# Kernel optimization log

Hardware: AMD Instinct MI355X
Metric: run time of the kernel (lower is better)

Reference implementation:

```python
import jax, jax.numpy as jnp
import numpy as np

N_COMP = 4        # config.n_components (num_cell_anchors = 1)
C = 256           # FPN channel width
ANCHOR_SCALE = 8.0  # anchor side = stride * 8 (single cell anchor per location)


def _conv(x, w, b, pad):
    y = jax.lax.conv_general_dilated(x, w, (1, 1), [(pad, pad), (pad, pad)],
                                     dimension_numbers=('NCHW', 'OIHW', 'NCHW'))
    return y + b[None, :, None, None]


def _anchors(H, W, stride):
    ys = (jnp.arange(H, dtype=jnp.float32) + 0.5) * stride
    xs = (jnp.arange(W, dtype=jnp.float32) + 0.5) * stride
    cy, cx = jnp.meshgrid(ys, xs, indexing='ij')
    s = stride * ANCHOR_SCALE * 0.5
    return jnp.stack([cx - s, cy - s, cx + s, cy + s], -1).reshape(-1, 4)


def _decode(anchors, deltas):
    # anchors [N,4] xyxy, deltas [B,N,4] -> boxes [B,N,4]
    aw = anchors[:, 2] - anchors[:, 0]
    ah = anchors[:, 3] - anchors[:, 1]
    acx = (anchors[:, 0] + anchors[:, 2]) * 0.5
    acy = (anchors[:, 1] + anchors[:, 3]) * 0.5
    cx = acx + deltas[..., 0] * aw
    cy = acy + deltas[..., 1] * ah
    bw = aw * jnp.exp(jnp.clip(deltas[..., 2], -10.0, 10.0))
    bh = ah * jnp.exp(jnp.clip(deltas[..., 3], -10.0, 10.0))
    return jnp.stack([cx - bw * 0.5, cy - bh * 0.5, cx + bw * 0.5, cy + bh * 0.5], -1)


def _forward(feats, im_info, w_qy1, b_qy1, w_qy2, b_qy2, w_qy, b_qy,
             w_rpn, b_rpn, w_cls, b_cls, w_mean, b_mean):
    strides = [64.0, 32.0, 16.0, 8.0, 4.0]  # off_stride = 2**(L-1) halving per level, base_stride=4
    outs = []
    for x, stride in zip(feats, strides):
        h = jax.nn.relu(_conv(x, w_qy1, b_qy1, 1))
        h = jax.nn.relu(_conv(h, w_qy2, b_qy2, 1))
        qy = _conv(h, w_qy, b_qy, 1)                 # [B, K, H, W]
        mix = jax.nn.softmax(qy, axis=1)             # per-location component weights
        bb_c, sc_c = [], []
        for n in range(N_COMP):
            # one-hot component indicator map concatenated onto the feature
            y = jnp.zeros_like(qy).at[:, n].set(1.0)
            t = jax.nn.relu(_conv(jnp.concatenate([x, y], axis=1), w_rpn, b_rpn, 1))
            sc_c.append(_conv(t, w_cls, b_cls, 0))    # [B,2,H,W]
            bb_c.append(_conv(t, w_mean, b_mean, 0))  # [B,4,H,W]; eval: bbox = mean
        # find_top_rpn_gmm_box: combine components with qy softmax weights
        bb = (mix[:, :, None] * jnp.stack(bb_c, 1)).sum(1)   # [B,4,H,W]
        sc = (mix[:, :, None] * jnp.stack(sc_c, 1)).sum(1)   # [B,2,H,W]
        B, _, H, W = bb.shape
        deltas = bb.transpose(0, 2, 3, 1).reshape(B, H * W, 4)
        scores = sc.transpose(0, 2, 3, 1).reshape(B, H * W, 2)
        boxes = _decode(_anchors(H, W, stride), deltas)
        lim = jnp.stack([im_info[:, 1], im_info[:, 0], im_info[:, 1], im_info[:, 0]], -1)[:, None, :]
        boxes = jnp.clip(boxes, 0.0, lim)             # clip to image
        outs.append(jnp.concatenate([boxes, scores], -1))
    return jnp.concatenate(outs, axis=1)  # [B, sum(H*W), 6]


def setup_inputs() -> dict:
    key = jax.random.key(0)
    ks = jax.random.split(key, 12)
    fshapes = [(2, C, 13, 19), (2, C, 25, 38), (2, C, 50, 76), (2, C, 100, 152), (2, C, 200, 304)]
    inp = {f"feat{i}": jax.random.normal(ks[i], s, jnp.float32) for i, s in enumerate(fshapes)}
    inp["im_info"] = jnp.tile(jnp.array([[800.0, 1216.0, 1.0, 800.0, 1216.0, 1.0]], jnp.float32), (2, 1))
    std = 0.01
    inp["w_qy1"] = jax.random.normal(ks[5], (C, C, 3, 3), jnp.float32) * std
    inp["b_qy1"] = jnp.zeros((C,), jnp.float32)
    inp["w_qy2"] = jax.random.normal(ks[6], (C, C, 3, 3), jnp.float32) * std
    inp["b_qy2"] = jnp.zeros((C,), jnp.float32)
    inp["w_qy"] = jax.random.normal(ks[7], (N_COMP, C, 3, 3), jnp.float32) * std
    inp["b_qy"] = jnp.zeros((N_COMP,), jnp.float32)
    inp["w_rpn"] = jax.random.normal(ks[8], (C, C + N_COMP, 3, 3), jnp.float32) * std
    inp["b_rpn"] = jnp.zeros((C,), jnp.float32)
    inp["w_cls"] = jax.random.normal(ks[9], (2, C, 1, 1), jnp.float32) * std
    inp["b_cls"] = jnp.zeros((2,), jnp.float32)
    inp["w_mean"] = jax.random.normal(ks[10], (4, C, 1, 1), jnp.float32) * std
    inp["b_mean"] = jnp.zeros((4,), jnp.float32)
    return inp


def reference(feat0, feat1, feat2, feat3, feat4, im_info,
              w_qy1, b_qy1, w_qy2, b_qy2, w_qy, b_qy,
              w_rpn, b_rpn, w_cls, b_cls, w_mean, b_mean):
    return _forward([feat0, feat1, feat2, feat3, feat4], im_info,
                    w_qy1, b_qy1, w_qy2, b_qy2, w_qy, b_qy,
                    w_rpn, b_rpn, w_cls, b_cls, w_mean, b_mean)
```

## Files before the change

kernel.cpp:

```cpp
#include <hip/hip_runtime.h>
#include <math.h>


typedef __attribute__((ext_vector_type(8))) short short8;
typedef __attribute__((ext_vector_type(4))) float f32x4;

#define TOT 80997

struct Tab {
    int tilesX[5];
    int blkBase[6];
    int H[5];
    int W5[5];
    int poff[6];
    int cvtBase[6];
};

static __device__ __forceinline__ ushort f2bf(float f) {
    union { float f; unsigned u; } x; x.f = f;
    unsigned r = (x.u + 0x7FFFu + ((x.u >> 16) & 1u)) >> 16;
    return (ushort)r;
}
static __device__ __forceinline__ float bf2f(ushort u) {
    union { unsigned u; float f; } x; x.u = ((unsigned)u) << 16;
    return x.f;
}

static __device__ __forceinline__ void gl_lds16(const ushort* g, ushort* l) {
    __builtin_amdgcn_global_load_lds(
        (const __attribute__((address_space(1))) void*)g,
        (__attribute__((address_space(3))) void*)l, 16, 0, 0);
}

__global__ __launch_bounds__(256) void cvtT_kernel(
    const float* __restrict__ f0, const float* __restrict__ f1,
    const float* __restrict__ f2, const float* __restrict__ f3,
    const float* __restrict__ f4, ushort* __restrict__ xn, Tab tab)
{
    __shared__ __align__(16) ushort s[64 * 264];
    const int tid = threadIdx.x;
    int t = blockIdx.x, L = 0;
    while (t >= tab.cvtBase[L + 1]) ++L;
    const int tile = t - tab.cvtBase[L];
    const int HW = tab.H[L] * tab.W5[L];
    const int pos0 = tile * 64;
    const int b = blockIdx.z;
    const float* fs[5] = {f0, f1, f2, f3, f4};
    const float* xp = fs[L] + (size_t)b * 256 * HW;

    const int p = tid & 63;
    const int icr = tid >> 6;
    const int pos = pos0 + p;
    for (int ic4 = 0; ic4 < 256; ic4 += 4) {
        const int ic = ic4 + icr;
        float v = 0.f;
        if (pos < HW) v = xp[(size_t)ic * HW + pos];
        s[p * 264 + ic] = f2bf(v);
    }
    __syncthreads();
    const int seg = tid & 31;
    for (int k = 0; k < 8; ++k) {
        const int pp = (tid >> 5) + k * 8;
        const int gpos = pos0 + pp;
        if (gpos < HW) {
            short8 v = *(const short8*)&s[pp * 264 + seg * 8];
            __builtin_nontemporal_store(v,
                (short8*)(xn + ((size_t)b * TOT + tab.poff[L] + gpos) * 256 + seg * 8));
        }
    }
}

__global__ __launch_bounds__(256) void pack_w_kernel(
    const float* __restrict__ w, ushort* __restrict__ pw, int icfull)
{
    int idx = blockIdx.x * 256 + threadIdx.x;
    if (idx >= 589824) return;
    const int within = idx & 511;
    const int lm  = within >> 5;
    const int qe  = within & 31;
    const int rest = idx >> 9;
    const int ocg = rest & 15;
    const int tc  = rest >> 4;
    const int c   = tc & 7;
    const int tap = tc >> 3;
    const int oc = ocg * 16 + lm;
    const int ic = c * 32 + qe;
    pw[idx] = f2bf(w[((size_t)oc * icfull + ic) * 9 + tap]);
}

__global__ __launch_bounds__(256) void pack_qy_kernel(
    const float* __restrict__ wqy, ushort* __restrict__ pwqy)
{
    int idx = blockIdx.x * 256 + threadIdx.x;
    if (idx >= 9216) return;
    int ic = idx & 255;
    int t  = (idx >> 8) % 9;
    int n  = (idx >> 8) / 9;
    pwqy[idx] = f2bf(wqy[n * 2304 + ic * 9 + t]);
}

__global__ __launch_bounds__(256) void btabT_kernel(
    const float* __restrict__ w_rpn, float* __restrict__ btabT)
{
    int idx = blockIdx.x * 256 + threadIdx.x;
    if (idx >= 2304) return;
    const int oc = idx & 255;
    const int cs = idx >> 8;
    const int cy = cs / 3, cx = cs % 3;
    float4 o;
    float* op = (float*)&o;
    for (int n = 0; n < 4; ++n) {
        float s = 0.f;
        for (int ky = 0; ky < 3; ++ky) {
            if (cy == 0 && ky == 0) continue;
            if (cy == 2 && ky == 2) continue;
            for (int kx = 0; kx < 3; ++kx) {
                if (cx == 0 && kx == 0) continue;
                if (cx == 2 && kx == 2) continue;
                s += w_rpn[(size_t)oc * 2340 + (256 + n) * 9 + ky * 3 + kx];
            }
        }
        op[n] = s;
    }
    ((float4*)btabT)[cs * 256 + oc] = o;
}

__global__ void pack_head_kernel(const float* __restrict__ w_cls,
                                 const float* __restrict__ w_mean,
                                 float* __restrict__ wcp, float* __restrict__ wmp,
                                 ushort* __restrict__ zpg)
{
    const int oc = threadIdx.x;
    wcp[oc * 2]     = w_cls[oc];
    wcp[oc * 2 + 1] = w_cls[256 + oc];
    float4 m;
    m.x = w_mean[oc];       m.y = w_mean[256 + oc];
    m.z = w_mean[512 + oc]; m.w = w_mean[768 + oc];
    ((float4*)wmp)[oc] = m;
    if (oc < 32) zpg[oc] = 0;
}

__global__ __launch_bounds__(512, 2) void conv3x3_mfma(
    const ushort* __restrict__ inN,
    const ushort* __restrict__ pw0, const ushort* __restrict__ pw1,
    const float* __restrict__ bias0, const float* __restrict__ bias1,
    ushort* __restrict__ out0, ushort* __restrict__ out1,
    const ushort* __restrict__ zpg,
    int jobs, int reluFlags, Tab tab)
{
    __shared__ __align__(16) ushort smem[62976];
    ushort* s_out = smem + 46080;

    const int tid = threadIdx.x;
    const int nper = (int)(gridDim.x >> 3);
    const int id = ((int)blockIdx.x & 7) * nper + ((int)blockIdx.x >> 3);

    const int bsum = tab.blkBase[5];
    const int bb = (id >= bsum) ? 1 : 0;
    int t = id - bsum * bb;
    int L = 0;
    while (t >= tab.blkBase[L + 1]) ++L;
    const int rel = t - tab.blkBase[L];
    const int tX = tab.tilesX[L];
    const int H = tab.H[L], W = tab.W5[L];
    const int y0 = (rel / tX) * 8;
    const int x0 = (rel % tX) * 16;
    const int poff = tab.poff[L];

    const int lane = tid & 63;
    const int wave = tid >> 6;
    const int lm   = lane & 15;
    const int quad = lane >> 4;

    const size_t inBase = ((size_t)bb * TOT + poff) * 256;

    {
        const int c = wave;
#pragma unroll
        for (int kk = 0; kk < 10; ++kk) {
            const int ug = kk * 4;
            const int yi = y0 - 1 + kk;
            const int xi = x0 + lm;
            const ushort* src = zpg;
            if (yi >= 0 && yi < H && xi < W)
                src = inN + inBase + ((size_t)yi * W + xi) * 256 + c * 32 + quad * 8;
            gl_lds16(src, &smem[(c * 40 + ug) * 128]);
        }
    }
    auto haloStage = [&](int pbase) {
        const int p = pbase + lane;
        const int c = p / 80;
        const int rem = p - c * 80;
        const int r = rem >> 3;
        const int icb = (rem >> 1) & 3;
        const int side = rem & 1;
        const int yi = y0 - 1 + r;
        const int xi = side ? (x0 + 16) : (x0 - 1);
        const ushort* src = zpg;
        if (yi >= 0 && yi < H && xi >= 0 && xi < W)
            src = inN + inBase + ((size_t)yi * W + xi) * 256 + c * 32 + icb * 8;
        gl_lds16(src, &smem[40960 + pbase * 8]);
    };
    haloStage(wave * 64);
    if (wave < 2) haloStage(512 + wave * 64);
    __syncthreads();

#pragma unroll 1
    for (int job = 0; job < jobs; ++job) {
        const ushort* pwj  = job ? pw1 : pw0;
        const float*  bsj  = job ? bias1 : bias0;
        ushort*       outj = job ? out1 : out0;
        const int relu = (reluFlags >> job) & 1;
        const ushort* pwl = pwj + (size_t)(wave * 2) * 512 + lm * 32 + quad * 8;

        f32x4 acc[2][8];
#pragma unroll
        for (int i = 0; i < 2; ++i)
#pragma unroll
            for (int j = 0; j < 8; ++j)
                acc[i][j] = (f32x4){0.f, 0.f, 0.f, 0.f};

#pragma unroll 1
        for (int c = 0; c < 8; ++c) {
#pragma unroll
            for (int kx = 0; kx < 3; ++kx) {
                short8 av[3][2];
#pragma unroll
                for (int ky = 0; ky < 3; ++ky) {
                    const ushort* pa = pwl + (size_t)((ky * 3 + kx) * 8 + c) * 8192;
                    av[ky][0] = *(const short8*)(pa);
                    av[ky][1] = *(const short8*)(pa + 512);
                }
                short8 bv[10];
#pragma unroll
                for (int r = 0; r < 10; ++r) {
                    const int u = r * 4 + quad;
                    const int lmx = lm + kx - 1;
                    int addr = ((c * 40 + u) * 16 + lmx) * 8;
                    if (kx == 0 && lm == 0)
                        addr = 40960 + (c * 80 + r * 8 + quad * 2 + 0) * 8;
                    if (kx == 2 && lm == 15)
                        addr = 40960 + (c * 80 + r * 8 + quad * 2 + 1) * 8;
                    bv[r] = *(const short8*)&smem[addr];
                }
#pragma unroll
                for (int ky = 0; ky < 3; ++ky)
#pragma unroll
                    for (int i = 0; i < 2; ++i)
#pragma unroll
                        for (int j = 0; j < 8; ++j)
                            acc[i][j] = __builtin_amdgcn_mfma_f32_16x16x32_bf16(
                                av[ky][i], bv[j + ky], acc[i][j], 0, 0, 0);
            }
        }

        auto epi = [&](const int ph) {
            __syncthreads();
#pragma unroll
            for (int i = 0; i < 2; ++i) {
                const int ocl = wave * 32 + i * 16 + quad * 4;
                const float4 b4 = *(const float4*)(bsj + ocl);
#pragma unroll
                for (int j4 = 0; j4 < 4; ++j4) {
                    const f32x4 a = acc[i][ph * 4 + j4];
                    const int p2 = j4 * 16 + lm;
                    float v0 = a[0] + b4.x;
                    float v1 = a[1] + b4.y;
                    float v2 = a[2] + b4.z;
                    float v3 = a[3] + b4.w;
                    if (relu) {
                        v0 = fmaxf(v0, 0.f); v1 = fmaxf(v1, 0.f);
                        v2 = fmaxf(v2, 0.f); v3 = fmaxf(v3, 0.f);
                    }
                    ushort4 o;
                    o.x = f2bf(v0); o.y = f2bf(v1); o.z = f2bf(v2); o.w = f2bf(v3);
                    *(ushort4*)&s_out[p2 * 264 + ocl] = o;
                }
            }
            __syncthreads();
#pragma unroll
            for (int it = 0; it < 4; ++it) {
                const int idx = it * 512 + tid;
                const int p2  = idx >> 5;
                const int sgm = idx & 31;
                const int r = ph * 4 + (p2 >> 4);
                const int y = y0 + r, x = x0 + (p2 & 15);
                if (y < H && x < W) {
                    short8 w = *(const short8*)&s_out[p2 * 264 + sgm * 8];
                    __builtin_nontemporal_store(w,
                        (short8*)(outj + ((size_t)bb * TOT + poff
                                  + (size_t)y * W + x) * 256 + sgm * 8));
                }
            }
        };
        epi(0);
        epi(1);
    }
}

__global__ __launch_bounds__(256) void qy_softmax_kernel(
    const ushort* __restrict__ h2, const ushort* __restrict__ pwqy,
    const float* __restrict__ bqy, float* __restrict__ mixv, Tab tab)
{
    const int tid = threadIdx.x;
    const int p = blockIdx.x * 64 + (tid >> 2);
    if (p >= TOT) return;
    const int q = tid & 3;
    const int b = blockIdx.z;
    int L = 0; while (p >= tab.poff[L + 1]) ++L;
    const int pos = p - tab.poff[L];
    const int W = tab.W5[L], H = tab.H[L];
    const int y = pos / W, x = pos - y * W;

    int  off[9];
    bool val[9];
#pragma unroll
    for (int ky = 0; ky < 3; ++ky)
#pragma unroll
        for (int kx = 0; kx < 3; ++kx) {
            const int t = ky * 3 + kx;
            const int yi = y + ky - 1, xi = x + kx - 1;
            val[t] = (yi >= 0 && yi < H && xi >= 0 && xi < W);
            off[t] = ((ky - 1) * W + (kx - 1)) * 256;
        }

    float a0 = 0.f, a1 = 0.f, a2 = 0.f, a3 = 0.f;
    const ushort* hp = h2 + ((size_t)b * TOT + p) * 256;
#pragma unroll 1
    for (int k = 0; k < 8; ++k) {
        const int sb = (k * 4 + q) * 8;
#pragma unroll
        for (int t = 0; t < 9; ++t) {
            if (!val[t]) continue;
            const short8 h8 = *(const short8*)(hp + off[t] + sb);
            float hv[8];
#pragma unroll
            for (int e = 0; e < 8; ++e) hv[e] = bf2f((ushort)h8[e]);
            const short8 w0 = *(const short8*)(pwqy + (0 * 9 + t) * 256 + sb);
            const short8 w1 = *(const short8*)(pwqy + (1 * 9 + t) * 256 + sb);
            const short8 w2 = *(const short8*)(pwqy + (2 * 9 + t) * 256 + sb);
            const short8 w3 = *(const short8*)(pwqy + (3 * 9 + t) * 256 + sb);
#pragma unroll
            for (int e = 0; e < 8; ++e) {
                a0 = fmaf(bf2f((ushort)w0[e]), hv[e], a0);
                a1 = fmaf(bf2f((ushort)w1[e]), hv[e], a1);
                a2 = fmaf(bf2f((ushort)w2[e]), hv[e], a2);
                a3 = fmaf(bf2f((ushort)w3[e]), hv[e], a3);
            }
        }
    }
    a0 += __shfl_xor(a0, 1); a0 += __shfl_xor(a0, 2);
    a1 += __shfl_xor(a1, 1); a1 += __shfl_xor(a1, 2);
    a2 += __shfl_xor(a2, 1); a2 += __shfl_xor(a2, 2);
    a3 += __shfl_xor(a3, 1); a3 += __shfl_xor(a3, 2);
    if (q == 0) {
        a0 += bqy[0]; a1 += bqy[1]; a2 += bqy[2]; a3 += bqy[3];
        const float mx = fmaxf(fmaxf(a0, a1), fmaxf(a2, a3));
        const float e0 = expf(a0 - mx), e1 = expf(a1 - mx);
        const float e2 = expf(a2 - mx), e3 = expf(a3 - mx);
        const float s = 1.f / (e0 + e1 + e2 + e3);
        float4 o; o.x = e0 * s; o.y = e1 * s; o.z = e2 * s; o.w = e3 * s;
        ((float4*)mixv)[(size_t)b * TOT + p] = o;
    }
}

__global__ __launch_bounds__(256) void final_kernel(
    const float* __restrict__ mixv, const ushort* __restrict__ U,
    const float* __restrict__ btabT,
    const float* __restrict__ wcp, const float* __restrict__ wmp,
    const float* __restrict__ b_cls, const float* __restrict__ b_mean,
    const float* __restrict__ im_info,
    float* __restrict__ outp, Tab tab)
{
    const int tid = threadIdx.x;
    const int p = blockIdx.x * 64 + (tid >> 2);
    if (p >= TOT) return;
    const int q = tid & 3;
    const int b = blockIdx.z;
    int L = 0; while (p >= tab.poff[L + 1]) ++L;
    const int pos = p - tab.poff[L];
    const int W = tab.W5[L], H = tab.H[L];
    const int y = pos / W, x = pos - y * W;
    const int cy = (y == 0) ? 0 : ((y == H - 1) ? 2 : 1);
    const int cx = (x == 0) ? 0 : ((x == W - 1) ? 2 : 1);
    const float* bT = btabT + (size_t)(cy * 3 + cx) * 1024;

    const float4 mm = ((const float4*)mixv)[(size_t)b * TOT + p];
    const ushort* up = U + ((size_t)b * TOT + p) * 256;

    float sc0 = 0.f, sc1 = 0.f, D0 = 0.f, D1 = 0.f, D2 = 0.f, D3 = 0.f;
#pragma unroll 1
    for (int k = 0; k < 8; ++k) {
        const int seg = k * 4 + q;
        const short8 u8 = *(const short8*)(up + seg * 8);
#pragma unroll
        for (int e = 0; e < 8; ++e) {
            const int oc = seg * 8 + e;
            const float u = bf2f((ushort)u8[e]);
            const float4 bt = *(const float4*)(bT + oc * 4);
            float T =      mm.x * fmaxf(u + bt.x, 0.f);
            T = fmaf(mm.y, fmaxf(u + bt.y, 0.f), T);
            T = fmaf(mm.z, fmaxf(u + bt.z, 0.f), T);
            T = fmaf(mm.w, fmaxf(u + bt.w, 0.f), T);
            const float2 wc = *(const float2*)(wcp + oc * 2);
            const float4 wm = *(const float4*)(wmp + oc * 4);
            sc0 = fmaf(wc.x, T, sc0); sc1 = fmaf(wc.y, T, sc1);
            D0 = fmaf(wm.x, T, D0);   D1 = fmaf(wm.y, T, D1);
            D2 = fmaf(wm.z, T, D2);   D3 = fmaf(wm.w, T, D3);
        }
    }
    sc0 += __shfl_xor(sc0, 1); sc0 += __shfl_xor(sc0, 2);
    sc1 += __shfl_xor(sc1, 1); sc1 += __shfl_xor(sc1, 2);
    D0  += __shfl_xor(D0, 1);  D0  += __shfl_xor(D0, 2);
    D1  += __shfl_xor(D1, 1);  D1  += __shfl_xor(D1, 2);
    D2  += __shfl_xor(D2, 1);  D2  += __shfl_xor(D2, 2);
    D3  += __shfl_xor(D3, 1);  D3  += __shfl_xor(D3, 2);

    if (q == 0) {
        sc0 += b_cls[0]; sc1 += b_cls[1];
        D0 += b_mean[0]; D1 += b_mean[1]; D2 += b_mean[2]; D3 += b_mean[3];
        const float stride_ = (float)(64 >> L);
        const float aw  = stride_ * 8.f;
        const float acx = (x + 0.5f) * stride_;
        const float acy = (y + 0.5f) * stride_;
        const float cxx = acx + D0 * aw;
        const float cyy = acy + D1 * aw;
        const float e2 = fminf(fmaxf(D2, -10.f), 10.f);
        const float e3 = fminf(fmaxf(D3, -10.f), 10.f);
        const float bw = aw * expf(e2);
        const float bh = aw * expf(e3);
        const float imH = im_info[b * 6 + 0], imW = im_info[b * 6 + 1];
        const float x1 = fminf(fmaxf(cxx - 0.5f * bw, 0.f), imW);
        const float y1 = fminf(fmaxf(cyy - 0.5f * bh, 0.f), imH);
        const float x2 = fminf(fmaxf(cxx + 0.5f * bw, 0.f), imW);
        const float y2 = fminf(fmaxf(cyy + 0.5f * bh, 0.f), imH);
        float* op = outp + ((size_t)b * TOT + p) * 6;
        float2 w01; w01.x = x1; w01.y = y1;
        float2 w23; w23.x = x2; w23.y = y2;
        float2 w45; w45.x = sc0; w45.y = sc1;
        ((float2*)op)[0] = w01; ((float2*)op)[1] = w23; ((float2*)op)[2] = w45;
    }
}

extern "C" void kernel_launch(void* const* d_in, const int* in_sizes, int n_in,
                              void* d_out, int out_size, void* d_ws, size_t ws_size,
                              hipStream_t stream)
{
    (void)in_sizes; (void)n_in; (void)out_size; (void)ws_size;

    const float* im_info = (const float*)d_in[5];
    const float* w_qy1 = (const float*)d_in[6];
    const float* b_qy1 = (const float*)d_in[7];
    const float* w_qy2 = (const float*)d_in[8];
    const float* b_qy2 = (const float*)d_in[9];
    const float* w_qy  = (const float*)d_in[10];
    const float* b_qy  = (const float*)d_in[11];
    const float* w_rpn = (const float*)d_in[12];
    const float* b_rpn = (const float*)d_in[13];
    const float* w_cls = (const float*)d_in[14];
    const float* b_cls = (const float*)d_in[15];
    const float* w_mean= (const float*)d_in[16];
    const float* b_mean= (const float*)d_in[17];
    float* out = (float*)d_out;

    Tab tab;
    const int Hs[5]  = {13, 25, 50, 100, 200};
    const int Ws5[5] = {19, 38, 76, 152, 304};
    int bsum = 0, psum = 0, csum = 0;
    for (int L = 0; L < 5; ++L) {
        tab.H[L] = Hs[L]; tab.W5[L] = Ws5[L];
        tab.tilesX[L] = (Ws5[L] + 15) / 16;
        tab.blkBase[L] = bsum;
        bsum += tab.tilesX[L] * ((Hs[L] + 7) / 8);
        tab.poff[L] = psum;
        tab.cvtBase[L] = csum;
        const int HW = Hs[L] * Ws5[L];
        psum += HW;
        csum += (HW + 63) / 64;
    }
    tab.blkBase[5] = bsum; tab.poff[5] = psum; tab.cvtBase[5] = csum;

    const size_t BIGE = (size_t)2 * TOT * 256;
    ushort* XBF  = (ushort*)d_ws;
    ushort* H1   = XBF + BIGE;
    ushort* U    = H1 + BIGE;
    ushort* H2   = XBF;
    float*  MIXv = (float*)(U + BIGE);
    float*  btabT= MIXv + (size_t)2 * TOT * 4;
    float*  wcp  = btabT + 9216;
    float*  wmp  = wcp + 512;
    ushort* PW1  = (ushort*)(wmp + 1024);
    ushort* PW2  = PW1 + 589824;
    ushort* PWR  = PW2 + 589824;
    ushort* PWQY = PWR + 589824;
    ushort* ZPG  = PWQY + 9216;

    cvtT_kernel<<<dim3(csum, 1, 2), 256, 0, stream>>>(
        (const float*)d_in[0], (const float*)d_in[1], (const float*)d_in[2],
        (const float*)d_in[3], (const float*)d_in[4], XBF, tab);
    pack_w_kernel<<<2304, 256, 0, stream>>>(w_qy1, PW1, 256);
    pack_w_kernel<<<2304, 256, 0, stream>>>(w_qy2, PW2, 256);
    pack_w_kernel<<<2304, 256, 0, stream>>>(w_rpn, PWR, 260);
    pack_qy_kernel<<<36, 256, 0, stream>>>(w_qy, PWQY);
    btabT_kernel<<<9, 256, 0, stream>>>(w_rpn, btabT);
    pack_head_kernel<<<1, 256, 0, stream>>>(w_cls, w_mean, wcp, wmp, ZPG);

    conv3x3_mfma<<<dim3(bsum * 2, 1, 1), 512, 0, stream>>>(
        XBF, PW1, PWR, b_qy1, b_rpn, H1, U, ZPG, 2, 0b01, tab);

    conv3x3_mfma<<<dim3(bsum * 2, 1, 1), 512, 0, stream>>>(
        H1, PW2, PW2, b_qy2, b_qy2, H2, H2, ZPG, 1, 0b1, tab);

    qy_softmax_kernel<<<dim3((TOT + 63) / 64, 1, 2), 256, 0, stream>>>(
        H2, PWQY, b_qy, MIXv, tab);

    final_kernel<<<dim3((TOT + 63) / 64, 1, 2), 256, 0, stream>>>(
        MIXv, U, btabT, wcp, wmp, b_cls, b_mean, im_info, out, tab);
}
```

Baseline: 1.171 ms.

## Split conv tile rows across two wave groups and XOR-swizzle LDS tile

Each conv block now runs 16 waves instead of 8. Waves are split into 8 channel slices times 2 row halves, so each wave accumulates 4 row positions instead of 8, which halves its accumulator registers and raises occupancy. The staged input tile in LDS is XOR-swizzled by quad to cut bank conflicts on the B-operand reads. In exchange, every wave now loads the same weight fragments twice per block and the epilogue needs per-half gating. The launch bound of 1024 threads with min 4 blocks forces tight register limits and risks spills.

```diff
diff --git a/kernel.cpp b/kernel.cpp
--- a/kernel.cpp
+++ b/kernel.cpp
@@ -140,7 +140,7 @@
     if (oc < 32) zpg[oc] = 0;
 }
 
-__global__ __launch_bounds__(512, 2) void conv3x3_mfma(
+__global__ __launch_bounds__(1024, 4) void conv3x3_mfma(
     const ushort* __restrict__ inN,
     const ushort* __restrict__ pw0, const ushort* __restrict__ pw1,
     const float* __restrict__ bias0, const float* __restrict__ bias1,
@@ -171,24 +171,26 @@
     const int wave = tid >> 6;
     const int lm   = lane & 15;
     const int quad = lane >> 4;
+    const int slice = wave & 7;
+    const int rh    = wave >> 3;
 
     const size_t inBase = ((size_t)bb * TOT + poff) * 256;
 
     {
-        const int c = wave;
-#pragma unroll
-        for (int kk = 0; kk < 10; ++kk) {
-            const int ug = kk * 4;
+        const int c = slice;
+#pragma unroll
+        for (int tt = 0; tt < 5; ++tt) {
+            const int kk = rh * 5 + tt;
             const int yi = y0 - 1 + kk;
-            const int xi = x0 + lm;
+            const int xi = x0 + (lm ^ quad);
             const ushort* src = zpg;
             if (yi >= 0 && yi < H && xi < W)
                 src = inN + inBase + ((size_t)yi * W + xi) * 256 + c * 32 + quad * 8;
-            gl_lds16(src, &smem[(c * 40 + ug) * 128]);
-        }
-    }
-    auto haloStage = [&](int pbase) {
-        const int p = pbase + lane;
+            gl_lds16(src, &smem[(c * 40 + kk * 4) * 128]);
+        }
+    }
+    if (wave < 10) {
+        const int p = wave * 64 + lane;
         const int c = p / 80;
         const int rem = p - c * 80;
         const int r = rem >> 3;
@@ -199,10 +201,8 @@
         const ushort* src = zpg;
         if (yi >= 0 && yi < H && xi >= 0 && xi < W)
             src = inN + inBase + ((size_t)yi * W + xi) * 256 + c * 32 + icb * 8;
-        gl_lds16(src, &smem[40960 + pbase * 8]);
-    };
-    haloStage(wave * 64);
-    if (wave < 2) haloStage(512 + wave * 64);
+        gl_lds16(src, &smem[40960 + wave * 64 * 8]);
+    }
     __syncthreads();
 
 #pragma unroll 1
@@ -211,13 +211,13 @@
         const float*  bsj  = job ? bias1 : bias0;
         ushort*       outj = job ? out1 : out0;
         const int relu = (reluFlags >> job) & 1;
-        const ushort* pwl = pwj + (size_t)(wave * 2) * 512 + lm * 32 + quad * 8;
-
-        f32x4 acc[2][8];
+        const ushort* pwl = pwj + (size_t)(slice * 2) * 512 + lm * 32 + quad * 8;
+
+        f32x4 acc[2][4];
 #pragma unroll
         for (int i = 0; i < 2; ++i)
 #pragma unroll
-            for (int j = 0; j < 8; ++j)
+            for (int j = 0; j < 4; ++j)
                 acc[i][j] = (f32x4){0.f, 0.f, 0.f, 0.f};
 
 #pragma unroll 1
@@ -231,24 +231,25 @@
                     av[ky][0] = *(const short8*)(pa);
                     av[ky][1] = *(const short8*)(pa + 512);
                 }
-                short8 bv[10];
-#pragma unroll
-                for (int r = 0; r < 10; ++r) {
+                short8 bv[6];
+#pragma unroll
+                for (int rr = 0; rr < 6; ++rr) {
+                    const int r = rh * 4 + rr;
                     const int u = r * 4 + quad;
                     const int lmx = lm + kx - 1;
-                    int addr = ((c * 40 + u) * 16 + lmx) * 8;
+                    int addr = ((c * 40 + u) * 16 + (lmx ^ quad)) * 8;
                     if (kx == 0 && lm == 0)
                         addr = 40960 + (c * 80 + r * 8 + quad * 2 + 0) * 8;
                     if (kx == 2 && lm == 15)
                         addr = 40960 + (c * 80 + r * 8 + quad * 2 + 1) * 8;
-                    bv[r] = *(const short8*)&smem[addr];
+                    bv[rr] = *(const short8*)&smem[addr];
                 }
 #pragma unroll
                 for (int ky = 0; ky < 3; ++ky)
 #pragma unroll
                     for (int i = 0; i < 2; ++i)
 #pragma unroll
-                        for (int j = 0; j < 8; ++j)
+                        for (int j = 0; j < 4; ++j)
                             acc[i][j] = __builtin_amdgcn_mfma_f32_16x16x32_bf16(
                                 av[ky][i], bv[j + ky], acc[i][j], 0, 0, 0);
             }
@@ -256,31 +257,34 @@
 
         auto epi = [&](const int ph) {
             __syncthreads();
-#pragma unroll
-            for (int i = 0; i < 2; ++i) {
-                const int ocl = wave * 32 + i * 16 + quad * 4;
-                const float4 b4 = *(const float4*)(bsj + ocl);
-#pragma unroll
-                for (int j4 = 0; j4 < 4; ++j4) {
-                    const f32x4 a = acc[i][ph * 4 + j4];
-                    const int p2 = j4 * 16 + lm;
-                    float v0 = a[0] + b4.x;
-                    float v1 = a[1] + b4.y;
-                    float v2 = a[2] + b4.z;
-                    float v3 = a[3] + b4.w;
-                    if (relu) {
-                        v0 = fmaxf(v0, 0.f); v1 = fmaxf(v1, 0.f);
-                        v2 = fmaxf(v2, 0.f); v3 = fmaxf(v3, 0.f);
+            if (rh == ph) {
+#pragma unroll
+                for (int i = 0; i < 2; ++i) {
+                    const int ocl = slice * 32 + i * 16 + quad * 4;
+                    const float4 b4 = *(const float4*)(bsj + ocl);
+#pragma unroll
+                    for (int j = 0; j < 4; ++j) {
+                        const f32x4 a = acc[i][j];
+                        const int p2 = j * 16 + lm;
+                        float v0 = a[0] + b4.x;
+                        float v1 = a[1] + b4.y;
+                        float v2 = a[2] + b4.z;
+                        float v3 = a[3] + b4.w;
+                        if (relu) {
+                            v0 = fmaxf(v0, 0.f); v1 = fmaxf(v1, 0.f);
+                            v2 = fmaxf(v2, 0.f); v3 = fmaxf(v3, 0.f);
+                        }
+                        ushort4 o;
+                        o.x = f2bf(v0); o.y = f2bf(v1);
+                        o.z = f2bf(v2); o.w = f2bf(v3);
+                        *(ushort4*)&s_out[p2 * 264 + ocl] = o;
                     }
-                    ushort4 o;
-                    o.x = f2bf(v0); o.y = f2bf(v1); o.z = f2bf(v2); o.w = f2bf(v3);
-                    *(ushort4*)&s_out[p2 * 264 + ocl] = o;
                 }
             }
             __syncthreads();
 #pragma unroll
-            for (int it = 0; it < 4; ++it) {
-                const int idx = it * 512 + tid;
+            for (int it = 0; it < 2; ++it) {
+                const int idx = it * 1024 + tid;
                 const int p2  = idx >> 5;
                 const int sgm = idx & 31;
                 const int r = ph * 4 + (p2 >> 4);
@@ -505,10 +509,10 @@
     btabT_kernel<<<9, 256, 0, stream>>>(w_rpn, btabT);
     pack_head_kernel<<<1, 256, 0, stream>>>(w_cls, w_mean, wcp, wmp, ZPG);
 
-    conv3x3_mfma<<<dim3(bsum * 2, 1, 1), 512, 0, stream>>>(
+    conv3x3_mfma<<<dim3(bsum * 2, 1, 1), 1024, 0, stream>>>(
         XBF, PW1, PWR, b_qy1, b_rpn, H1, U, ZPG, 2, 0b01, tab);
 
-    conv3x3_mfma<<<dim3(bsum * 2, 1, 1), 512, 0, stream>>>(
+    conv3x3_mfma<<<dim3(bsum * 2, 1, 1), 1024, 0, stream>>>(
         H1, PW2, PW2, b_qy2, b_qy2, H2, H2, ZPG, 1, 0b1, tab);
 
     qy_softmax_kernel<<<dim3((TOT + 63) / 64, 1, 2), 256, 0, stream>>>(
```

Result: slower. 1.308 ms (+11.7%).
